# Kernel tuning notes

Hardware: AMD Instinct MI355X
Metric: run time of the kernel (lower is better)

## Reference

```python
import jax, jax.numpy as jnp
import numpy as np

T = 2048          # num tokens (prefill)
H = 4096          # hidden_size
NH = 32           # num query heads
NKV = 8           # num kv heads (GQA)
HD = H // NH      # head_dim = 128
BASE = 1000000.0  # rope_theta
NEG = -1e30


def _rope(x, positions):
    # NeoX-style rotary embedding (vLLM default). x: [T, nh, HD]
    half = HD // 2
    inv_freq = 1.0 / (BASE ** (jnp.arange(half, dtype=jnp.float32) / half))
    freqs = positions.astype(jnp.float32)[:, None] * inv_freq  # [T, half]
    cos = jnp.concatenate([jnp.cos(freqs), jnp.cos(freqs)], -1)[:, None, :]
    sin = jnp.concatenate([jnp.sin(freqs), jnp.sin(freqs)], -1)[:, None, :]
    rot = jnp.concatenate([-x[..., half:], x[..., :half]], -1)
    return x * cos + rot * sin


def setup_inputs() -> dict:
    key = jax.random.key(0)
    k1, k2, k3 = jax.random.split(key, 3)
    hidden_states = jax.random.normal(k1, (T, H), jnp.float32)
    wqkv = jax.random.normal(k2, (H, (NH + 2 * NKV) * HD), jnp.float32) * 0.02
    wo = jax.random.normal(k3, (NH * HD, H), jnp.float32) * 0.02
    positions = jnp.arange(T, dtype=jnp.int32)
    return {"positions": positions, "hidden_states": hidden_states,
            "wqkv": wqkv, "wo": wo}


def reference(positions, hidden_states, wqkv, wo):
    # fused QKV projection
    qkv = hidden_states @ wqkv                      # [T, (NH+2*NKV)*HD]
    q, k, v = jnp.split(qkv, [NH * HD, NH * HD + NKV * HD], axis=-1)
    q = q.reshape(T, NH, HD)
    k = k.reshape(T, NKV, HD)
    v = v.reshape(T, NKV, HD)
    # inline RoPE on q, k
    q = _rope(q, positions)
    k = _rope(k, positions)
    # GQA: expand kv heads to query heads
    rep = NH // NKV
    k = jnp.repeat(k, rep, axis=1)                  # [T, NH, HD]
    v = jnp.repeat(v, rep, axis=1)
    # causal scaled dot-product attention (prefill path of PagedAttention)
    scores = jnp.einsum('qhd,khd->hqk', q, k) * (HD ** -0.5)  # [NH, T, T]
    causal = positions[:, None] >= positions[None, :]          # [T, T]
    scores = jnp.where(causal[None, :, :], scores, NEG)
    probs = jax.nn.softmax(scores, axis=-1)
    attn = jnp.einsum('hqk,khd->qhd', probs, v).reshape(T, NH * HD)
    return attn @ wo
```

## Files before the change

### kernel.cpp

```cpp
#include <hip/hip_runtime.h>
#include <hip/hip_bf16.h>

typedef __attribute__((ext_vector_type(8))) short bf16x8;
typedef __attribute__((ext_vector_type(4))) float f32x4;
typedef unsigned short u16;

#define T_TOK 2048
#define HID 4096
#define NH 32
#define NKV 8
#define HD 128
#define QKVN 6144
#define KOFF 4096
#define VOFF 5120
#define ATTN_SCALE 0.08838834764831845f

static __device__ __forceinline__ float bf2f(u16 x) {
    union { float f; unsigned u; } v; v.u = ((unsigned)x) << 16; return v.f;
}
static __device__ __forceinline__ u16 f2bf(float f) {
    union { float f; unsigned u; } v; v.f = f;
    unsigned u = v.u;
    unsigned r = (u + 0x7fff + ((u >> 16) & 1)) >> 16;
    return (u16)r;
}

static __device__ __forceinline__ void gload16(const u16* g, u16* l) {
    __builtin_amdgcn_global_load_lds((const __attribute__((address_space(1))) void*)g,
                                     (__attribute__((address_space(3))) void*)l, 16, 0, 0);
}

#define VMC(n) asm volatile("s_waitcnt vmcnt(%0)" :: "i"(n) : "memory")

__global__ __launch_bounds__(256) void convk(const float* __restrict__ in, u16* __restrict__ out) {
    int i = blockIdx.x * 256 + threadIdx.x;
    float4 v = ((const float4*)in)[i];
    ushort4 o;
    o.x = f2bf(v.x); o.y = f2bf(v.y); o.z = f2bf(v.z); o.w = f2bf(v.w);
    ((ushort4*)out)[i] = o;
}

__global__ __launch_bounds__(256) void transpk(const float* __restrict__ in, u16* __restrict__ out,
                                               int R, int C) {
    __shared__ float tile[64][65];
    int c0 = blockIdx.x * 64, r0 = blockIdx.y * 64;
    int tid = threadIdx.x;
#pragma unroll
    for (int it = 0; it < 4; ++it) {
        int ci = it * 256 + tid;
        int r = ci >> 4, c4 = (ci & 15) * 4;
        float4 v = *(const float4*)&in[(size_t)(r0 + r) * C + c0 + c4];
        tile[r][c4 + 0] = v.x; tile[r][c4 + 1] = v.y; tile[r][c4 + 2] = v.z; tile[r][c4 + 3] = v.w;
    }
    __syncthreads();
#pragma unroll
    for (int it = 0; it < 4; ++it) {
        int ci = it * 256 + tid;
        int c = ci >> 4, rq = (ci & 15) * 4;
        ushort4 o;
        o.x = f2bf(tile[rq + 0][c]); o.y = f2bf(tile[rq + 1][c]);
        o.z = f2bf(tile[rq + 2][c]); o.w = f2bf(tile[rq + 3][c]);
        *(ushort4*)&out[(size_t)(c0 + c) * R + r0 + rq] = o;
    }
}

template <int BN, int OUTF32>
__global__ __launch_bounds__(512) void gemm8p(const u16* __restrict__ A, const u16* __restrict__ Bt,
                                              void* __restrict__ Cout, int M, int N, int K) {
    constexpr int BM = 256, BK = 32;
    constexpr int WN = BN / 4;
    constexpr int NF = WN / 16;
    constexpr int BCH = BN / 16;
    constexpr int CA = 2 + (BCH + 7) / 8;
    constexpr int CB = 2 + BCH / 8;
    constexpr int ABUF = BM * BK;
    constexpr int BBUF = BN * BK;
    constexpr int BUFSZ = ABUF + BBUF;

    __shared__ __attribute__((aligned(16))) u16 lds[4 * BUFSZ];

    int bid = blockIdx.x;
    int m0 = (bid & 7) * BM, n0 = (bid >> 3) * BN;
    int tid = threadIdx.x, lane = tid & 63, wid = tid >> 6;
    int wm = wid >> 2, wn = wid & 3;
    int l15 = lane & 15, g4 = lane >> 4;
    int srow = lane >> 2;
    int sslot = (lane & 3) ^ ((lane >> 3) & 3);
    int swz = (g4 ^ ((l15 >> 1) & 3)) * 8;
    int NK = K / BK;
    bool shortw = (CA != CB) && (wid >= 4);

    auto STAGE = [&](int kt, int c) {
        u16* base = &lds[(kt & 3) * BUFSZ];
        size_t kcol = (size_t)kt * BK + sslot * 8;
        if (c < 2) {
            int ch = wid * 2 + c;
            gload16(&A[(size_t)(m0 + ch * 16 + srow) * K + kcol], base + ch * 512);
        } else {
            int ch = (c - 2) * 8 + wid;
            if (ch < BCH)
                gload16(&Bt[(size_t)(n0 + ch * 16 + srow) * K + kcol], base + ABUF + ch * 512);
        }
    };

    f32x4 acc[8][NF];
#pragma unroll
    for (int i = 0; i < 8; ++i)
#pragma unroll
        for (int j = 0; j < NF; ++j) acc[i][j] = (f32x4){0.f, 0.f, 0.f, 0.f};

    for (int t = 0; t < 3; ++t)
        for (int c = 0; c < CA; ++c) STAGE(t, c);
    if (shortw) VMC(2 * CB); else VMC(2 * CA);
    __builtin_amdgcn_s_barrier();
    __builtin_amdgcn_sched_barrier(0);

    for (int g = 0; g < NK; ++g) {
        const u16* ab = &lds[(g & 3) * BUFSZ];
        const u16* bb = ab + ABUF;

        bf16x8 bfr[NF], af[4];
#pragma unroll
        for (int j = 0; j < NF; ++j)
            bfr[j] = *(const bf16x8*)&bb[(wn * WN + j * 16 + l15) * BK + swz];
#pragma unroll
        for (int i = 0; i < 4; ++i)
            af[i] = *(const bf16x8*)&ab[(wm * 128 + i * 16 + l15) * BK + swz];
        if (g + 3 < NK) {
            STAGE(g + 3, 0); STAGE(g + 3, 1);
        }
        __builtin_amdgcn_s_setprio(1);
#pragma unroll
        for (int i = 0; i < 4; ++i)
#pragma unroll
            for (int j = 0; j < NF; ++j)
                acc[i][j] = __builtin_amdgcn_mfma_f32_16x16x32_bf16(af[i], bfr[j], acc[i][j], 0, 0, 0);
        __builtin_amdgcn_s_setprio(0);

        bf16x8 af2[4];
#pragma unroll
        for (int i = 0; i < 4; ++i)
            af2[i] = *(const bf16x8*)&ab[(wm * 128 + (4 + i) * 16 + l15) * BK + swz];
        if (g + 3 < NK) {
#pragma unroll
            for (int c = 2; c < CA; ++c) STAGE(g + 3, c);
        }
        __builtin_amdgcn_s_setprio(1);
#pragma unroll
        for (int i = 0; i < 4; ++i)
#pragma unroll
            for (int j = 0; j < NF; ++j)
                acc[4 + i][j] = __builtin_amdgcn_mfma_f32_16x16x32_bf16(af2[i], bfr[j], acc[4 + i][j], 0, 0, 0);
        __builtin_amdgcn_s_setprio(0);

        if (g < NK - 3)       { if (shortw) VMC(2 * CB); else VMC(2 * CA); }
        else if (g == NK - 3) { if (shortw) VMC(CB);     else VMC(CA); }
        else if (g == NK - 2) VMC(0);
        __builtin_amdgcn_s_barrier();
        __builtin_amdgcn_sched_barrier(0);
    }

#pragma unroll
    for (int mi = 0; mi < 8; ++mi)
#pragma unroll
        for (int j = 0; j < NF; ++j)
#pragma unroll
            for (int i = 0; i < 4; ++i) {
                int row = m0 + wm * 128 + mi * 16 + g4 * 4 + i;
                int col = n0 + wn * WN + j * 16 + l15;
                float v = acc[mi][j][i];
                if (OUTF32) ((float*)Cout)[(size_t)row * N + col] = v;
                else        ((u16*)Cout)[(size_t)row * N + col] = f2bf(v);
            }
}

__global__ __launch_bounds__(256) void ropek(u16* __restrict__ qkvb, const int* __restrict__ positions) {
    __shared__ float cs_[64], sn_[64];
    int t = blockIdx.x;
    float pos = (float)positions[t];
    if (threadIdx.x < 64) {
        int d = threadIdx.x;
        float inv = exp2f(-(float)d * (19.931568569324174f / 64.0f));
        float fr = pos * inv;
        cs_[d] = cosf(fr);
        sn_[d] = sinf(fr);
    }
    __syncthreads();
#pragma unroll
    for (int it = 0; it < 10; ++it) {
        int ci = it * 256 + threadIdx.x;
        int hh = ci >> 6, d = ci & 63;
        int base = (hh < NH) ? hh * HD : KOFF + (hh - NH) * HD;
        size_t off = (size_t)t * QKVN + base + d;
        float x1 = bf2f(qkvb[off]);
        float x2 = bf2f(qkvb[off + 64]);
        float s = sn_[d], c = cs_[d];
        float y1 = x1 * c - x2 * s;
        float y2 = x2 * c + x1 * s;
        if (hh < NH) { y1 *= ATTN_SCALE; y2 *= ATTN_SCALE; }
        qkvb[off]      = f2bf(y1);
        qkvb[off + 64] = f2bf(y2);
    }
}

__global__ __launch_bounds__(256) void vtranspk(const u16* __restrict__ qkvb, u16* __restrict__ vT) {
    __shared__ __attribute__((aligned(16))) u16 tile[64][136];
    int kvh = blockIdx.x, t0 = blockIdx.y * 64;
    int tid = threadIdx.x;
#pragma unroll
    for (int it = 0; it < 4; ++it) {
        int ci = it * 256 + tid;
        int r = ci >> 4, c8 = (ci & 15) * 8;
        *(bf16x8*)&tile[r][c8] = *(const bf16x8*)&qkvb[(size_t)(t0 + r) * QKVN + VOFF + kvh * HD + c8];
    }
    __syncthreads();
#pragma unroll
    for (int it = 0; it < 4; ++it) {
        int ci = it * 256 + tid;
        int d = ci >> 3, tc = (ci & 7) * 8;
        union { bf16x8 v; u16 u[8]; } o;
#pragma unroll
        for (int e = 0; e < 8; ++e) o.u[e] = tile[tc + e][d];
        *(bf16x8*)&vT[((size_t)kvh * HD + d) * T_TOK + t0 + tc] = o.v;
    }
}

__global__ __launch_bounds__(512) void attnk(const u16* __restrict__ qkvb, const u16* __restrict__ vT,
                                             u16* __restrict__ attnb) {
    __shared__ __attribute__((aligned(16))) u16 kt_[64 * 136];
    __shared__ __attribute__((aligned(16))) u16 vt_[128 * 72];
    __shared__ __attribute__((aligned(16))) u16 pl_[8 * 16 * 72];
    int h = blockIdx.x, qt = 15 - blockIdx.y;
    int kvh = h >> 2;
    int q0 = qt * 128;
    int tid = threadIdx.x, lane = tid & 63, wid = tid >> 6;
    int l15 = lane & 15, g = lane >> 4;

    const u16* kbase = qkvb + KOFF + (size_t)kvh * HD;
    const u16* vbase = vT + (size_t)kvh * HD * T_TOK;

    bf16x8 qf[4];
    int qrow = q0 + wid * 16 + l15;
#pragma unroll
    for (int ks = 0; ks < 4; ++ks)
        qf[ks] = *(const bf16x8*)&qkvb[(size_t)qrow * QKVN + h * HD + ks * 32 + g * 8];

    f32x4 o[8];
#pragma unroll
    for (int df = 0; df < 8; ++df) o[df] = (f32x4){0.f, 0.f, 0.f, 0.f};
    float m_run[4], l_run[4];
#pragma unroll
    for (int i = 0; i < 4; ++i) { m_run[i] = -3.0e38f; l_run[i] = 0.f; }

    int NT = 2 * qt + 2;

    bf16x8 kreg[2], vreg[2];
#pragma unroll
    for (int it = 0; it < 2; ++it) {
        int gi = it * 512 + tid;
        kreg[it] = *(const bf16x8*)&kbase[(size_t)(gi >> 4) * QKVN + (gi & 15) * 8];
        vreg[it] = *(const bf16x8*)&vbase[(size_t)(gi >> 3) * T_TOK + (gi & 7) * 8];
    }
#pragma unroll
    for (int it = 0; it < 2; ++it) {
        int gi = it * 512 + tid;
        *(bf16x8*)&kt_[(gi >> 4) * 136 + (gi & 15) * 8] = kreg[it];
        *(bf16x8*)&vt_[(gi >> 3) * 72 + (gi & 7) * 8] = vreg[it];
    }
#pragma unroll
    for (int it = 0; it < 2; ++it) {
        int gi = it * 512 + tid;
        kreg[it] = *(const bf16x8*)&kbase[(size_t)(64 + (gi >> 4)) * QKVN + (gi & 15) * 8];
        vreg[it] = *(const bf16x8*)&vbase[(size_t)(gi >> 3) * T_TOK + 64 + (gi & 7) * 8];
    }
    __syncthreads();

    for (int kt2 = 0; kt2 < NT; ++kt2) {
        int kvb = kt2 * 64;
        bool active = (kvb <= q0 + wid * 16 + 15);
        bool diag   = (kvb + 63 > q0 + wid * 16);

        if (active) {
            f32x4 s[4];
#pragma unroll
            for (int nf = 0; nf < 4; ++nf) s[nf] = (f32x4){0.f, 0.f, 0.f, 0.f};
            __builtin_amdgcn_s_setprio(1);
#pragma unroll
            for (int ks = 0; ks < 4; ++ks) {
#pragma unroll
                for (int nf = 0; nf < 4; ++nf) {
                    bf16x8 bfr = *(const bf16x8*)&kt_[(nf * 16 + l15) * 136 + ks * 32 + g * 8];
                    s[nf] = __builtin_amdgcn_mfma_f32_16x16x32_bf16(qf[ks], bfr, s[nf], 0, 0, 0);
                }
            }
            __builtin_amdgcn_s_setprio(0);

            float mrow[4];
#pragma unroll
            for (int i = 0; i < 4; ++i) {
                int qr = q0 + wid * 16 + g * 4 + i;
                float mx = -3.0e38f;
#pragma unroll
                for (int nf = 0; nf < 4; ++nf) {
                    float v = s[nf][i];
                    if (diag) {
                        int kvc = kvb + nf * 16 + l15;
                        v = (kvc <= qr) ? v : -1.0e30f;
                        s[nf][i] = v;
                    }
                    mx = fmaxf(mx, v);
                }
                mrow[i] = mx;
            }
#pragma unroll
            for (int dd = 1; dd < 16; dd <<= 1)
#pragma unroll
                for (int i = 0; i < 4; ++i) mrow[i] = fmaxf(mrow[i], __shfl_xor(mrow[i], dd));

            int ok = 1;
#pragma unroll
            for (int i = 0; i < 4; ++i) ok &= (mrow[i] <= m_run[i] + 8.0f) ? 1 : 0;
            if (!__all(ok)) {
                float alpha[4];
#pragma unroll
                for (int i = 0; i < 4; ++i) {
                    float mnew = fmaxf(m_run[i], mrow[i]);
                    alpha[i] = __expf(m_run[i] - mnew);
                    m_run[i] = mnew;
                    l_run[i] *= alpha[i];
                }
#pragma unroll
                for (int df = 0; df < 8; ++df)
#pragma unroll
                    for (int i = 0; i < 4; ++i) o[df][i] *= alpha[i];
            }

            float rsum[4] = {0.f, 0.f, 0.f, 0.f};
#pragma unroll
            for (int nf = 0; nf < 4; ++nf)
#pragma unroll
                for (int i = 0; i < 4; ++i) {
                    float p = __expf(s[nf][i] - m_run[i]);
                    rsum[i] += p;
                    pl_[wid * 1152 + (g * 4 + i) * 72 + nf * 16 + l15] = f2bf(p);
                }
#pragma unroll
            for (int dd = 1; dd < 16; dd <<= 1)
#pragma unroll
                for (int i = 0; i < 4; ++i) rsum[i] += __shfl_xor(rsum[i], dd);
#pragma unroll
            for (int i = 0; i < 4; ++i) l_run[i] += rsum[i];

            __builtin_amdgcn_s_setprio(1);
#pragma unroll
            for (int ks2 = 0; ks2 < 2; ++ks2) {
                bf16x8 af = *(const bf16x8*)&pl_[wid * 1152 + l15 * 72 + ks2 * 32 + g * 8];
#pragma unroll
                for (int df = 0; df < 8; ++df) {
                    bf16x8 bfr = *(const bf16x8*)&vt_[(df * 16 + l15) * 72 + ks2 * 32 + g * 8];
                    o[df] = __builtin_amdgcn_mfma_f32_16x16x32_bf16(af, bfr, o[df], 0, 0, 0);
                }
            }
            __builtin_amdgcn_s_setprio(0);
        }

        if (kt2 < NT - 1) {
            __syncthreads();
#pragma unroll
            for (int it = 0; it < 2; ++it) {
                int gi = it * 512 + tid;
                *(bf16x8*)&kt_[(gi >> 4) * 136 + (gi & 15) * 8] = kreg[it];
                *(bf16x8*)&vt_[(gi >> 3) * 72 + (gi & 7) * 8] = vreg[it];
            }
            int ktl = (kt2 + 2 < NT) ? kt2 + 2 : NT - 1;
#pragma unroll
            for (int it = 0; it < 2; ++it) {
                int gi = it * 512 + tid;
                kreg[it] = *(const bf16x8*)&kbase[(size_t)(ktl * 64 + (gi >> 4)) * QKVN + (gi & 15) * 8];
                vreg[it] = *(const bf16x8*)&vbase[(size_t)(gi >> 3) * T_TOK + ktl * 64 + (gi & 7) * 8];
            }
            __syncthreads();
        }
    }

#pragma unroll
    for (int df = 0; df < 8; ++df)
#pragma unroll
        for (int i = 0; i < 4; ++i) {
            int qr = q0 + wid * 16 + g * 4 + i;
            int col = h * HD + df * 16 + l15;
            attnb[(size_t)qr * (NH * HD) + col] = f2bf(o[df][i] / l_run[i]);
        }
}

extern "C" void kernel_launch(void* const* d_in, const int* in_sizes, int n_in,
                              void* d_out, int out_size, void* d_ws, size_t ws_size,
                              hipStream_t stream) {
    const int*   positions = (const int*)d_in[0];
    const float* hs        = (const float*)d_in[1];
    const float* wqkv      = (const float*)d_in[2];
    const float* wo        = (const float*)d_in[3];
    float* out = (float*)d_out;

    char* ws = (char*)d_ws;
    u16* hsb   = (u16*)(ws);
    u16* wqkvT = (u16*)(ws + 16777216);
    u16* woT   = (u16*)(ws + 16777216 + 50331648);
    u16* qkvb  = (u16*)(ws + 16777216 + 50331648 + 33554432);
    u16* vT    = (u16*)(ws + 16777216 + 50331648 + 33554432 + 25165824);
    u16* attnb = hsb;

    convk<<<8192, 256, 0, stream>>>(hs, hsb);
    transpk<<<dim3(96, 64), 256, 0, stream>>>(wqkv, wqkvT, HID, QKVN);
    transpk<<<dim3(64, 64), 256, 0, stream>>>(wo, woT, HID, HID);

    gemm8p<192, 0><<<dim3(256), 512, 0, stream>>>(hsb, wqkvT, qkvb, T_TOK, QKVN, HID);

    ropek<<<T_TOK, 256, 0, stream>>>(qkvb, positions);

    vtranspk<<<dim3(NKV, 32), 256, 0, stream>>>(qkvb, vT);

    attnk<<<dim3(NH, 16), 512, 0, stream>>>(qkvb, vT, attnb);

    gemm8p<128, 1><<<dim3(256), 512, 0, stream>>>(attnb, woT, out, T_TOK, HID, HID);
}
```

Measured before the change: 335.6 us.

## Rewrite GEMM as 128xBN tiles with BK=64 double-buffered four-phase pipeline

Replaces the 256xBN, BK=32, four-stage LDS ring GEMM with a 128-row by wider-column tile (384 for QKV, 256 for output) using BK=64 and two LDS buffers. Each K step is split into four MFMA phases separated by barriers, and the next tile's A and B halves are loaded in between those phases. The aim is to overlap global-to-LDS traffic with MFMA work more finely and to halve the number of K iterations. The cost is more barriers per iteration and a shallower prefetch depth, and the tile shape change alters how much operand data is reused.

```diff
diff --git a/kernel.cpp b/kernel.cpp
--- a/kernel.cpp
+++ b/kernel.cpp
@@ -31,6 +31,9 @@
 }
 
 #define VMC(n) asm volatile("s_waitcnt vmcnt(%0)" :: "i"(n) : "memory")
+#define LGKM0() asm volatile("s_waitcnt lgkmcnt(0)" ::: "memory")
+#define BAR() __builtin_amdgcn_s_barrier()
+#define SCHB() __builtin_amdgcn_sched_barrier(0)
 
 __global__ __launch_bounds__(256) void convk(const float* __restrict__ in, u16* __restrict__ out) {
     int i = blockIdx.x * 256 + threadIdx.x;
@@ -65,110 +68,124 @@
 }
 
 template <int BN, int OUTF32>
-__global__ __launch_bounds__(512) void gemm8p(const u16* __restrict__ A, const u16* __restrict__ Bt,
+__global__ __launch_bounds__(512) void gemm4p(const u16* __restrict__ A, const u16* __restrict__ Bt,
                                               void* __restrict__ Cout, int M, int N, int K) {
-    constexpr int BM = 256, BK = 32;
-    constexpr int WN = BN / 4;
-    constexpr int NF = WN / 16;
-    constexpr int BCH = BN / 16;
-    constexpr int CA = 2 + (BCH + 7) / 8;
-    constexpr int CB = 2 + BCH / 8;
-    constexpr int ABUF = BM * BK;
-    constexpr int BBUF = BN * BK;
-    constexpr int BUFSZ = ABUF + BBUF;
-
-    __shared__ __attribute__((aligned(16))) u16 lds[4 * BUFSZ];
+    constexpr int NF = BN / 64;
+    constexpr int LB = BN / 128;
+    constexpr int DBUF = (128 + BN) * 64;
+    constexpr int BHALF = (BN / 2) * 64;
+    __shared__ __attribute__((aligned(16))) u16 lds[2 * DBUF];
 
     int bid = blockIdx.x;
-    int m0 = (bid & 7) * BM, n0 = (bid >> 3) * BN;
+    int m0 = (bid & 15) * 128, n0 = (bid >> 4) * BN;
     int tid = threadIdx.x, lane = tid & 63, wid = tid >> 6;
     int wm = wid >> 2, wn = wid & 3;
     int l15 = lane & 15, g4 = lane >> 4;
-    int srow = lane >> 2;
-    int sslot = (lane & 3) ^ ((lane >> 3) & 3);
-    int swz = (g4 ^ ((l15 >> 1) & 3)) * 8;
-    int NK = K / BK;
-    bool shortw = (CA != CB) && (wid >= 4);
-
-    auto STAGE = [&](int kt, int c) {
-        u16* base = &lds[(kt & 3) * BUFSZ];
-        size_t kcol = (size_t)kt * BK + sslot * 8;
-        if (c < 2) {
-            int ch = wid * 2 + c;
-            gload16(&A[(size_t)(m0 + ch * 16 + srow) * K + kcol], base + ch * 512);
-        } else {
-            int ch = (c - 2) * 8 + wid;
-            if (ch < BCH)
-                gload16(&Bt[(size_t)(n0 + ch * 16 + srow) * K + kcol], base + ABUF + ch * 512);
-        }
+    int sw = l15 & 7;
+    int srow = tid >> 3;
+    int sslot8 = (((tid & 7) ^ ((tid >> 3) & 7))) * 8;
+    int brow0 = (wn & 1) * (BN / 4);
+    int NK = K / 64;
+
+    auto STAGE_A = [&](int kt, int h) {
+        gload16(&A[(size_t)(m0 + h * 64 + srow) * K + kt * 64 + sslot8],
+                &lds[(kt & 1) * DBUF + h * 4096 + wid * 512]);
     };
-
-    f32x4 acc[8][NF];
-#pragma unroll
-    for (int i = 0; i < 8; ++i)
+    auto STAGE_B = [&](int kt, int bh) {
+#pragma unroll
+        for (int it = 0; it < LB; ++it)
+            gload16(&Bt[(size_t)(n0 + bh * (BN / 2) + it * 64 + srow) * K + kt * 64 + sslot8],
+                    &lds[(kt & 1) * DBUF + 8192 + bh * BHALF + it * 4096 + wid * 512]);
+    };
+
+    f32x4 acc[4][NF];
+#pragma unroll
+    for (int i = 0; i < 4; ++i)
 #pragma unroll
         for (int j = 0; j < NF; ++j) acc[i][j] = (f32x4){0.f, 0.f, 0.f, 0.f};
 
-    for (int t = 0; t < 3; ++t)
-        for (int c = 0; c < CA; ++c) STAGE(t, c);
-    if (shortw) VMC(2 * CB); else VMC(2 * CA);
-    __builtin_amdgcn_s_barrier();
-    __builtin_amdgcn_sched_barrier(0);
+    STAGE_A(0, 0); STAGE_A(0, 1); STAGE_B(0, 0); STAGE_B(0, 1);
+    STAGE_A(1, 0); STAGE_A(1, 1); STAGE_B(1, 0); STAGE_B(1, 1);
+    VMC(2 + 2 * LB);
+    BAR(); SCHB();
 
     for (int g = 0; g < NK; ++g) {
-        const u16* ab = &lds[(g & 3) * BUFSZ];
-        const u16* bb = ab + ABUF;
-
-        bf16x8 bfr[NF], af[4];
-#pragma unroll
-        for (int j = 0; j < NF; ++j)
-            bfr[j] = *(const bf16x8*)&bb[(wn * WN + j * 16 + l15) * BK + swz];
-#pragma unroll
-        for (int i = 0; i < 4; ++i)
-            af[i] = *(const bf16x8*)&ab[(wm * 128 + i * 16 + l15) * BK + swz];
-        if (g + 3 < NK) {
-            STAGE(g + 3, 0); STAGE(g + 3, 1);
-        }
+        const u16* dd = &lds[(g & 1) * DBUF];
+        const u16* aw = dd + wm * 4096;
+        const u16* bw = dd + 8192 + (wn >> 1) * BHALF;
+        bool mid = (g > 0) && (g + 1 < NK);
+        bf16x8 bfr[NF], af0, af1;
+
+#pragma unroll
+        for (int nf = 0; nf < NF; ++nf)
+            bfr[nf] = *(const bf16x8*)&bw[(brow0 + nf * 16 + l15) * 64 + ((g4 ^ sw) * 8)];
+        af0 = *(const bf16x8*)&aw[(0 * 16 + l15) * 64 + ((g4 ^ sw) * 8)];
+        af1 = *(const bf16x8*)&aw[(1 * 16 + l15) * 64 + ((g4 ^ sw) * 8)];
+        if (mid) STAGE_A(g + 1, 0);
+        BAR(); LGKM0();
         __builtin_amdgcn_s_setprio(1);
 #pragma unroll
-        for (int i = 0; i < 4; ++i)
-#pragma unroll
-            for (int j = 0; j < NF; ++j)
-                acc[i][j] = __builtin_amdgcn_mfma_f32_16x16x32_bf16(af[i], bfr[j], acc[i][j], 0, 0, 0);
+        for (int nf = 0; nf < NF; ++nf) {
+            acc[0][nf] = __builtin_amdgcn_mfma_f32_16x16x32_bf16(af0, bfr[nf], acc[0][nf], 0, 0, 0);
+            acc[1][nf] = __builtin_amdgcn_mfma_f32_16x16x32_bf16(af1, bfr[nf], acc[1][nf], 0, 0, 0);
+        }
         __builtin_amdgcn_s_setprio(0);
-
-        bf16x8 af2[4];
-#pragma unroll
-        for (int i = 0; i < 4; ++i)
-            af2[i] = *(const bf16x8*)&ab[(wm * 128 + (4 + i) * 16 + l15) * BK + swz];
-        if (g + 3 < NK) {
-#pragma unroll
-            for (int c = 2; c < CA; ++c) STAGE(g + 3, c);
-        }
+        BAR();
+
+        af0 = *(const bf16x8*)&aw[(2 * 16 + l15) * 64 + ((g4 ^ sw) * 8)];
+        af1 = *(const bf16x8*)&aw[(3 * 16 + l15) * 64 + ((g4 ^ sw) * 8)];
+        if (mid) STAGE_B(g + 1, 1);
+        BAR(); LGKM0();
         __builtin_amdgcn_s_setprio(1);
 #pragma unroll
-        for (int i = 0; i < 4; ++i)
-#pragma unroll
-            for (int j = 0; j < NF; ++j)
-                acc[4 + i][j] = __builtin_amdgcn_mfma_f32_16x16x32_bf16(af2[i], bfr[j], acc[4 + i][j], 0, 0, 0);
+        for (int nf = 0; nf < NF; ++nf) {
+            acc[2][nf] = __builtin_amdgcn_mfma_f32_16x16x32_bf16(af0, bfr[nf], acc[2][nf], 0, 0, 0);
+            acc[3][nf] = __builtin_amdgcn_mfma_f32_16x16x32_bf16(af1, bfr[nf], acc[3][nf], 0, 0, 0);
+        }
         __builtin_amdgcn_s_setprio(0);
-
-        if (g < NK - 3)       { if (shortw) VMC(2 * CB); else VMC(2 * CA); }
-        else if (g == NK - 3) { if (shortw) VMC(CB);     else VMC(CA); }
+        BAR();
+
+#pragma unroll
+        for (int nf = 0; nf < NF; ++nf)
+            bfr[nf] = *(const bf16x8*)&bw[(brow0 + nf * 16 + l15) * 64 + (((4 + g4) ^ sw) * 8)];
+        af0 = *(const bf16x8*)&aw[(0 * 16 + l15) * 64 + (((4 + g4) ^ sw) * 8)];
+        af1 = *(const bf16x8*)&aw[(1 * 16 + l15) * 64 + (((4 + g4) ^ sw) * 8)];
+        if (mid) STAGE_A(g + 1, 1);
+        BAR(); LGKM0();
+        __builtin_amdgcn_s_setprio(1);
+#pragma unroll
+        for (int nf = 0; nf < NF; ++nf) {
+            acc[0][nf] = __builtin_amdgcn_mfma_f32_16x16x32_bf16(af0, bfr[nf], acc[0][nf], 0, 0, 0);
+            acc[1][nf] = __builtin_amdgcn_mfma_f32_16x16x32_bf16(af1, bfr[nf], acc[1][nf], 0, 0, 0);
+        }
+        __builtin_amdgcn_s_setprio(0);
+        BAR();
+
+        af0 = *(const bf16x8*)&aw[(2 * 16 + l15) * 64 + (((4 + g4) ^ sw) * 8)];
+        af1 = *(const bf16x8*)&aw[(3 * 16 + l15) * 64 + (((4 + g4) ^ sw) * 8)];
+        if (g + 2 < NK) STAGE_B(g + 2, 0);
+        BAR(); LGKM0();
+        __builtin_amdgcn_s_setprio(1);
+#pragma unroll
+        for (int nf = 0; nf < NF; ++nf) {
+            acc[2][nf] = __builtin_amdgcn_mfma_f32_16x16x32_bf16(af0, bfr[nf], acc[2][nf], 0, 0, 0);
+            acc[3][nf] = __builtin_amdgcn_mfma_f32_16x16x32_bf16(af1, bfr[nf], acc[3][nf], 0, 0, 0);
+        }
+        __builtin_amdgcn_s_setprio(0);
+        if (g <= NK - 3)      VMC(LB);
         else if (g == NK - 2) VMC(0);
-        __builtin_amdgcn_s_barrier();
-        __builtin_amdgcn_sched_barrier(0);
-    }
-
-#pragma unroll
-    for (int mi = 0; mi < 8; ++mi)
-#pragma unroll
-        for (int j = 0; j < NF; ++j)
+        BAR(); SCHB();
+    }
+
+#pragma unroll
+    for (int mf = 0; mf < 4; ++mf)
+#pragma unroll
+        for (int nf = 0; nf < NF; ++nf)
 #pragma unroll
             for (int i = 0; i < 4; ++i) {
-                int row = m0 + wm * 128 + mi * 16 + g4 * 4 + i;
-                int col = n0 + wn * WN + j * 16 + l15;
-                float v = acc[mi][j][i];
+                int row = m0 + wm * 64 + mf * 16 + g4 * 4 + i;
+                int col = n0 + wn * (BN / 4) + nf * 16 + l15;
+                float v = acc[mf][nf][i];
                 if (OUTF32) ((float*)Cout)[(size_t)row * N + col] = v;
                 else        ((u16*)Cout)[(size_t)row * N + col] = f2bf(v);
             }
@@ -414,7 +431,7 @@
     transpk<<<dim3(96, 64), 256, 0, stream>>>(wqkv, wqkvT, HID, QKVN);
     transpk<<<dim3(64, 64), 256, 0, stream>>>(wo, woT, HID, HID);
 
-    gemm8p<192, 0><<<dim3(256), 512, 0, stream>>>(hsb, wqkvT, qkvb, T_TOK, QKVN, HID);
+    gemm4p<384, 0><<<dim3(256), 512, 0, stream>>>(hsb, wqkvT, qkvb, T_TOK, QKVN, HID);
 
     ropek<<<T_TOK, 256, 0, stream>>>(qkvb, positions);
 
@@ -422,5 +439,5 @@
 
     attnk<<<dim3(NH, 16), 512, 0, stream>>>(qkvb, vT, attnb);
 
-    gemm8p<128, 1><<<dim3(256), 512, 0, stream>>>(attnb, woT, out, T_TOK, HID, HID);
-}
+    gemm4p<256, 1><<<dim3(256), 512, 0, stream>>>(attnb, woT, out, T_TOK, HID, HID);
+}
```

Result: no change. 334.0 us (-0.5%).
